# Optimization experiments

Measured on AMD Instinct MI355X. Metric: run time of the kernel, lower is better.

## Reference

```python
import jax, jax.numpy as jnp
import numpy as np

HIDDEN = 1024
HEADS = 8
HEAD = HIDDEN // HEADS
EPS = 1e-5


def _gammas():
    lo = np.log(1.0 / 512.0)
    hi = np.log(1.0 / 32.0)
    lin = np.linspace(lo, hi, HEADS)
    return jnp.asarray(1.0 - np.exp(lin), dtype=jnp.float32)  # [H]


def setup_inputs() -> dict:
    key = jax.random.key(0)
    ks = jax.random.split(key, 7)
    B, S = 2, 2048
    x = jax.random.normal(ks[0], (B, S, HIDDEN), dtype=jnp.float32)
    # Per-head retention projection weights (Retention(head_size, gamma)): [H, d, d]
    Wq = jax.random.normal(ks[1], (HEADS, HEAD, HEAD), dtype=jnp.float32) / HEAD
    Wk = jax.random.normal(ks[2], (HEADS, HEAD, HEAD), dtype=jnp.float32) / HEAD
    Wv = jax.random.normal(ks[3], (HEADS, HEAD, HEAD), dtype=jnp.float32) / HEAD
    W1 = jax.random.normal(ks[4], (HIDDEN, HIDDEN), dtype=jnp.float32) / HIDDEN
    W2 = jax.random.normal(ks[5], (HIDDEN, HIDDEN), dtype=jnp.float32) / HIDDEN
    gn_w = jnp.ones((HIDDEN,), dtype=jnp.float32)
    gn_b = jnp.zeros((HIDDEN,), dtype=jnp.float32)
    return {"x": x, "Wq": Wq, "Wk": Wk, "Wv": Wv, "W1": W1, "W2": W2,
            "gn_w": gn_w, "gn_b": gn_b}


def _decay_mask(S, gammas):
    idx = jnp.arange(S)
    diff = idx[:, None] - idx[None, :]              # [S, S]
    causal = diff >= 0
    safe = jnp.where(causal, diff, 0).astype(jnp.float32)
    D = jnp.where(causal[None], gammas[:, None, None] ** safe[None], 0.0)  # [H,S,S]
    return D


def _msr_forward(x, Wq, Wk, Wv, W1, W2, gn_w, gn_b):
    B, S, _ = x.shape
    xh = x.reshape(B, S, HEADS, HEAD)               # per-head slices
    q = jnp.einsum('bshd,hde->bshe', xh, Wq)
    k = jnp.einsum('bshd,hde->bshe', xh, Wk)
    v = jnp.einsum('bshd,hde->bshe', xh, Wv)
    D = _decay_mask(S, _gammas())                   # [H,S,S]
    scores = jnp.einsum('bnhd,bmhd->bhnm', q, k) * D[None]
    ret = jnp.einsum('bhnm,bmhd->bnhd', scores, v)  # [B,S,H,d]
    # GroupNorm(num_groups=H, channels=HIDDEN) over flattened rows
    mu = jnp.mean(ret, axis=-1, keepdims=True)
    var = jnp.var(ret, axis=-1, keepdims=True)
    ret = (ret - mu) * jax.lax.rsqrt(var + EPS)
    ret = ret.reshape(B, S, HIDDEN) * gn_w + gn_b
    gated = x @ W1
    out = gated * jax.nn.sigmoid(gated) + ret       # swish gate + residual add
    return out @ W2


def reference(x, Wq, Wk, Wv, W1, W2, gn_w, gn_b):
    return _msr_forward(x, Wq, Wk, Wv, W1, W2, gn_w, gn_b)
```

## Files before the change

kernel.cpp:

```cpp
#include <hip/hip_runtime.h>
#include <hip/hip_bf16.h>

#define HID 1024
#define NH 8
#define HD 128
#define BB 2
#define SS 2048
#define CHK 128
#define NCH 16

typedef __attribute__((ext_vector_type(8))) short short8;
typedef __attribute__((ext_vector_type(4))) float f32x4;

static __device__ __forceinline__ float b2f(unsigned short u){
  unsigned int x = ((unsigned int)u) << 16; float f;
  __builtin_memcpy(&f, &x, 4); return f;
}
static __device__ __forceinline__ unsigned short f2b(float f){
  unsigned int x; __builtin_memcpy(&x, &f, 4);
  x += 0x7fffu + ((x >> 16) & 1u);
  return (unsigned short)(x >> 16);
}
static __device__ __forceinline__ float head_gamma(int h){
  double lo = -6.238324625039508;
  double hi = -3.4657359027997265;
  double lin = lo + (hi - lo) * ((double)h / 7.0);
  return (float)(1.0 - exp(lin));
}
static __device__ __forceinline__ f32x4 MFMA(short8 a, short8 b, f32x4 c){
  return __builtin_amdgcn_mfma_f32_16x16x32_bf16(a, b, c, 0, 0, 0);
}

typedef const __attribute__((address_space(1))) unsigned int* gas1_u32p;
typedef __attribute__((address_space(3))) unsigned int* las3_u32p;
static __device__ __forceinline__ void gload_lds16(const void* g, void* l){
  __builtin_amdgcn_global_load_lds((gas1_u32p)g, (las3_u32p)l, 16, 0, 0);
}

__global__ void k_cvt(const float* __restrict__ in, unsigned short* __restrict__ out, int n){
  int i = (blockIdx.x*blockDim.x + threadIdx.x)*4;
  int st = gridDim.x*blockDim.x*4;
  for (; i < n; i += st){
    float4 v = *(const float4*)(in + i);
    unsigned short o[4] = { f2b(v.x), f2b(v.y), f2b(v.z), f2b(v.w) };
    *(uint2*)(out + i) = *(const uint2*)o;
  }
}

__global__ __launch_bounds__(256) void k_wT(const float* __restrict__ in,
                                            unsigned short* __restrict__ out,
                                            int R, int C){
  __shared__ float tile[32][33];
  in  += (size_t)blockIdx.z * R * C;
  out += (size_t)blockIdx.z * R * C;
  int c0 = blockIdx.x*32, r0 = blockIdx.y*32;
  int tx = threadIdx.x & 31, ty = threadIdx.x >> 5;
  #pragma unroll
  for (int i=0;i<4;i++) tile[ty+i*8][tx] = in[(size_t)(r0+ty+i*8)*C + c0+tx];
  __syncthreads();
  #pragma unroll
  for (int i=0;i<4;i++) out[(size_t)(c0+ty+i*8)*R + r0+tx] = f2b(tile[tx][ty+i*8]);
}

__global__ __launch_bounds__(256) void k_qkv(
    const unsigned short* __restrict__ xb,
    const unsigned short* __restrict__ wqT,
    const unsigned short* __restrict__ wkT,
    const unsigned short* __restrict__ wvT,
    unsigned short* __restrict__ qb,
    unsigned short* __restrict__ kb,
    unsigned short* __restrict__ vb)
{
  int bid = blockIdx.x;
  int stile = bid & 31;
  int bh = bid >> 5;
  int h = bh & 7, b = bh >> 3;
  int t = threadIdx.x, wv = t>>6, l = t&63, lr = l&15, lg = l>>4;
  int row0 = stile*64 + wv*16;
  short8 a[4];
  const unsigned short* xp = xb + (size_t)(b*SS + row0 + lr)*HID + h*HD + lg*8;
  #pragma unroll
  for (int kk=0;kk<4;kk++) a[kk] = *(const short8*)(xp + kk*32);
  size_t obase = ((size_t)bh*SS + row0)*HD;
  const unsigned short* wts[3] = { wqT + (size_t)h*HD*HD, wkT + (size_t)h*HD*HD, wvT + (size_t)h*HD*HD };
  unsigned short* outs[3]      = { qb + obase, kb + obase, vb + obase };
  for (int m=0;m<3;m++){
    const unsigned short* wb = wts[m];
    unsigned short* op = outs[m];
    #pragma unroll
    for (int nt=0;nt<8;nt++){
      f32x4 acc = {0.f,0.f,0.f,0.f};
      #pragma unroll
      for (int kk=0;kk<4;kk++){
        short8 bfr = *(const short8*)(wb + (size_t)(nt*16+lr)*HD + kk*32 + lg*8);
        acc = MFMA(a[kk], bfr, acc);
      }
      #pragma unroll
      for (int r=0;r<4;r++)
        op[(size_t)(lg*4+r)*HD + nt*16 + lr] = f2b(acc[r]);
    }
  }
}

__global__ __launch_bounds__(256) void k_chunksum(
    const unsigned short* __restrict__ kb,
    const unsigned short* __restrict__ vb,
    float* __restrict__ U)
{
  int bid = blockIdx.x;
  int c = bid & 15, bh = bid >> 4, h = bh & 7;
  float g = head_gamma(h);
  float l2g = log2f(g);
  __shared__ unsigned short kT[HD][72];
  __shared__ unsigned short vT[HD][72];
  int t = threadIdx.x, wv = t>>6, l = t&63, lr = l&15, lg = l>>4;
  const unsigned short* kc = kb + ((size_t)bh*SS + c*CHK)*HD;
  const unsigned short* vc = vb + ((size_t)bh*SS + c*CHK)*HD;
  f32x4 acc[2][8];
  #pragma unroll
  for (int i=0;i<2;i++)
    #pragma unroll
    for (int j=0;j<8;j++) acc[i][j] = (f32x4){0.f,0.f,0.f,0.f};
  for (int half=0; half<2; half++){
    if (half) __syncthreads();
    #pragma unroll
    for (int it=0; it<4; it++){
      int cid = t + it*256;
      int m = cid >> 4;
      int dc = (cid & 15)*8;
      int mg = half*64 + m;
      short8 kv = *(const short8*)(kc + (size_t)mg*HD + dc);
      short8 vv = *(const short8*)(vc + (size_t)mg*HD + dc);
      float ks = exp2f((float)(CHK-1-mg)*l2g);
      #pragma unroll
      for (int e=0;e<8;e++){
        kT[dc+e][m] = f2b(b2f((unsigned short)kv[e]) * ks);
        vT[dc+e][m] = (unsigned short)vv[e];
      }
    }
    __syncthreads();
    #pragma unroll
    for (int ks=0; ks<2; ks++){
      short8 bfr[8];
      #pragma unroll
      for (int nt=0;nt<8;nt++) bfr[nt] = *(const short8*)&kT[nt*16+lr][ks*32+lg*8];
      #pragma unroll
      for (int mt=0;mt<2;mt++){
        short8 afr = *(const short8*)&vT[wv*32+mt*16+lr][ks*32+lg*8];
        #pragma unroll
        for (int nt=0;nt<8;nt++)
          acc[mt][nt] = MFMA(afr, bfr[nt], acc[mt][nt]);
      }
    }
  }
  float* Up = U + (size_t)bid*HD*HD;
  #pragma unroll
  for (int mt=0;mt<2;mt++)
    #pragma unroll
    for (int nt=0;nt<8;nt++)
      #pragma unroll
      for (int r=0;r<4;r++)
        Up[(size_t)(wv*32+mt*16+lg*4+r)*HD + nt*16+lr] = acc[mt][nt][r];
}

__global__ __launch_bounds__(256) void k_state(
    const float* __restrict__ U,
    unsigned short* __restrict__ ST)
{
  int bid = blockIdx.x;
  int eb = bid & 63, bh = bid >> 6, h = bh & 7;
  float g = head_gamma(h);
  float d128 = exp2f(128.f * log2f(g));
  int idx = eb*256 + threadIdx.x;
  const float* Ub = U + (size_t)bh*NCH*HD*HD + idx;
  unsigned short* Sb = ST + (size_t)bh*NCH*HD*HD + idx;
  float s = 0.f;
  #pragma unroll
  for (int c=0;c<NCH;c++){
    Sb[(size_t)c*HD*HD] = f2b(s);
    s = s*d128 + Ub[(size_t)c*HD*HD];
  }
}

__global__ __launch_bounds__(256) void k_ret(
    const unsigned short* __restrict__ qb,
    const unsigned short* __restrict__ kb,
    const unsigned short* __restrict__ vb,
    const unsigned short* __restrict__ ST,
    const float* __restrict__ gnw,
    const float* __restrict__ gnb,
    unsigned short* __restrict__ ret)
{
  int bid = blockIdx.x;
  int j = bid & 15, bh = bid >> 4, h = bh & 7, b = bh >> 3;
  int p = j*CHK;
  float g = head_gamma(h);
  float l2g = log2f(g);
  __shared__ unsigned short sc[CHK][136];
  __shared__ unsigned short vT[HD][72];
  __shared__ float gpow[CHK];
  int t = threadIdx.x, wv = t>>6, l = t&63, lr = l&15, lg = l>>4;
  if (t < CHK) gpow[t] = exp2f((float)t * l2g);
  const unsigned short* qc = qb + ((size_t)bh*SS + p)*HD;
  const unsigned short* kc = kb + ((size_t)bh*SS + p)*HD;
  const unsigned short* vc = vb + ((size_t)bh*SS + p)*HD;
  const unsigned short* Sp = ST + (size_t)bid*HD*HD;
  __syncthreads();

  auto stageV = [&](int half){
    #pragma unroll
    for (int it=0; it<4; it++){
      int cid = t + it*256;
      int m = cid >> 4;
      int dc = (cid & 15)*8;
      short8 vv = *(const short8*)(vc + (size_t)(half*64 + m)*HD + dc);
      #pragma unroll
      for (int e=0;e<8;e++) vT[dc+e][m] = (unsigned short)vv[e];
    }
  };

  short8 qf[2][4];
  #pragma unroll
  for (int mt=0;mt<2;mt++)
    #pragma unroll
    for (int kk=0;kk<4;kk++)
      qf[mt][kk] = *(const short8*)(qc + (size_t)(wv*32+mt*16+lr)*HD + kk*32 + lg*8);

  #pragma unroll
  for (int nt=0;nt<8;nt++){
    f32x4 a0 = {0,0,0,0}, a1 = {0,0,0,0};
    #pragma unroll
    for (int kk=0;kk<4;kk++){
      short8 bfr = *(const short8*)(kc + (size_t)(nt*16+lr)*HD + kk*32 + lg*8);
      a0 = MFMA(qf[0][kk], bfr, a0);
      a1 = MFMA(qf[1][kk], bfr, a1);
    }
    int col = nt*16 + lr;
    #pragma unroll
    for (int r=0;r<4;r++){
      int r0 = wv*32 + lg*4 + r;
      int r1 = r0 + 16;
      float v0 = (col <= r0) ? a0[r]*gpow[r0-col] : 0.f;
      float v1 = (col <= r1) ? a1[r]*gpow[r1-col] : 0.f;
      sc[r0][col] = f2b(v0);
      sc[r1][col] = f2b(v1);
    }
  }
  stageV(0);
  __syncthreads();

  f32x4 acc[2][8];
  #pragma unroll
  for (int mt=0;mt<2;mt++)
    #pragma unroll
    for (int nt=0;nt<8;nt++){
      f32x4 a = {0,0,0,0};
      #pragma unroll
      for (int kk=0;kk<4;kk++){
        short8 bfr = *(const short8*)(Sp + (size_t)(nt*16+lr)*HD + kk*32 + lg*8);
        a = MFMA(qf[mt][kk], bfr, a);
      }
      acc[mt][nt] = a;
    }
  #pragma unroll
  for (int mt=0;mt<2;mt++)
    #pragma unroll
    for (int r=0;r<4;r++){
      int rr = wv*32 + mt*16 + lg*4 + r;
      float sf = gpow[rr]*g;
      #pragma unroll
      for (int nt=0;nt<8;nt++) acc[mt][nt][r] *= sf;
    }

  for (int half=0; half<2; half++){
    if (half){ __syncthreads(); stageV(1); __syncthreads(); }
    #pragma unroll
    for (int ks=0; ks<2; ks++){
      short8 bfr[8];
      #pragma unroll
      for (int nt=0;nt<8;nt++) bfr[nt] = *(const short8*)&vT[nt*16+lr][ks*32+lg*8];
      #pragma unroll
      for (int mt=0;mt<2;mt++){
        short8 afr = *(const short8*)&sc[wv*32+mt*16+lr][half*64 + ks*32 + lg*8];
        #pragma unroll
        for (int nt=0;nt<8;nt++)
          acc[mt][nt] = MFMA(afr, bfr[nt], acc[mt][nt]);
      }
    }
  }

  unsigned short* rp = ret + ((size_t)(b*SS + p))*HID + h*HD;
  const float* gw  = gnw + h*HD;
  const float* gbb = gnb + h*HD;
  #pragma unroll
  for (int mt=0;mt<2;mt++){
    #pragma unroll
    for (int r=0;r<4;r++){
      float s = 0.f, ss = 0.f;
      #pragma unroll
      for (int nt=0;nt<8;nt++){ float x = acc[mt][nt][r]; s += x; ss += x*x; }
      #pragma unroll
      for (int off=1; off<16; off<<=1){
        s  += __shfl_xor(s,  off, 64);
        ss += __shfl_xor(ss, off, 64);
      }
      float mu  = s*(1.f/128.f);
      float var = ss*(1.f/128.f) - mu*mu;
      float rs  = rsqrtf(var + 1e-5f);
      int rr = wv*32 + mt*16 + lg*4 + r;
      unsigned short* orow = rp + (size_t)rr*HID;
      #pragma unroll
      for (int nt=0;nt<8;nt++){
        int col = nt*16 + lr;
        orow[col] = f2b((acc[mt][nt][r]-mu)*rs*gw[col] + gbb[col]);
      }
    }
  }
}

template<int EPI>
__global__ __launch_bounds__(512) void k_gemm(
    const unsigned short* __restrict__ A,
    const unsigned short* __restrict__ BT,
    const unsigned short* __restrict__ radd,
    unsigned short* __restrict__ Cb,
    float* __restrict__ Cf,
    int M, int N, int K)
{
  __shared__ unsigned short ls[2][2][128*64];
  const int nb = N >> 7;
  const int m0 = (int)(blockIdx.x / nb) << 7;
  const int n0 = (int)(blockIdx.x % nb) << 7;
  const int t = threadIdx.x, wv = t>>6, l = t&63, lr = l&15, lg = l>>4;
  const int wr = (wv>>1)<<5;
  const int wc = (wv&1)<<6;
  const int srow = l >> 3;
  const int sgc  = ((l & 7) ^ srow) << 3;
  const unsigned short* Abase = A  + (size_t)(m0 + wv*16 + srow)*K + sgc;
  const unsigned short* Bbase = BT + (size_t)(n0 + wv*16 + srow)*K + sgc;

  auto stage = [&](int buf, int k0){
    unsigned short* la = &ls[buf][0][0];
    unsigned short* lb = &ls[buf][1][0];
    #pragma unroll
    for (int it=0; it<2; ++it){
      gload_lds16(Abase + (size_t)(it*8)*K + k0, la + (wv*16 + it*8)*64);
      gload_lds16(Bbase + (size_t)(it*8)*K + k0, lb + (wv*16 + it*8)*64);
    }
  };

  f32x4 acc[2][4];
  #pragma unroll
  for (int i=0;i<2;i++)
    #pragma unroll
    for (int j=0;j<4;j++) acc[i][j] = (f32x4){0,0,0,0};

  const int NT = K >> 6;
  stage(0, 0);
  __syncthreads();
  int cur = 0;
  for (int kt = 0; kt < NT; ++kt){
    if (kt+1 < NT) stage(cur^1, (kt+1)<<6);
    const unsigned short* pa = &ls[cur][0][0];
    const unsigned short* pb = &ls[cur][1][0];
    #pragma unroll
    for (int ks=0; ks<2; ++ks){
      short8 af[2], bf[4];
      #pragma unroll
      for (int i=0;i<2;i++){
        int ra = wr + i*16 + lr;
        af[i] = *(const short8*)(pa + ra*64 + ((((ks<<2)+lg) ^ (ra&7))<<3));
      }
      #pragma unroll
      for (int j=0;j<4;j++){
        int rb = wc + j*16 + lr;
        bf[j] = *(const short8*)(pb + rb*64 + ((((ks<<2)+lg) ^ (rb&7))<<3));
      }
      #pragma unroll
      for (int i=0;i<2;i++)
        #pragma unroll
        for (int j=0;j<4;j++)
          acc[i][j] = MFMA(af[i], bf[j], acc[i][j]);
    }
    __syncthreads();
    cur ^= 1;
  }

  #pragma unroll
  for (int i=0;i<2;i++){
    #pragma unroll
    for (int j=0;j<4;j++){
      #pragma unroll
      for (int r=0;r<4;r++){
        int row = m0 + wr + i*16 + lg*4 + r;
        int col = n0 + wc + j*16 + lr;
        float v = acc[i][j][r];
        if (EPI == 1){
          float sw = v / (1.f + __expf(-v));
          Cb[(size_t)row*N + col] = f2b(sw + b2f(radd[(size_t)row*N + col]));
        } else {
          Cf[(size_t)row*N + col] = v;
        }
      }
    }
  }
}

extern "C" void kernel_launch(void* const* d_in, const int* in_sizes, int n_in,
                              void* d_out, int out_size, void* d_ws, size_t ws_size,
                              hipStream_t stream)
{
  (void)in_sizes; (void)n_in; (void)out_size; (void)ws_size;
  const float* x   = (const float*)d_in[0];
  const float* Wq  = (const float*)d_in[1];
  const float* Wk  = (const float*)d_in[2];
  const float* Wv  = (const float*)d_in[3];
  const float* W1  = (const float*)d_in[4];
  const float* W2  = (const float*)d_in[5];
  const float* gnw = (const float*)d_in[6];
  const float* gnb = (const float*)d_in[7];
  float* out = (float*)d_out;

  char* wsp = (char*)d_ws;
  size_t off = 0;
  auto alloc = [&](size_t bytes)->void*{
    off = (off + 255) & ~(size_t)255;
    void* p = wsp + off; off += bytes; return p;
  };
  const size_t NTOK = (size_t)BB*SS;
  unsigned short* xb  = (unsigned short*)alloc(NTOK*HID*2);
  unsigned short* w1T = (unsigned short*)alloc((size_t)HID*HID*2);
  unsigned short* w2T = (unsigned short*)alloc((size_t)HID*HID*2);
  unsigned short* wqT = (unsigned short*)alloc((size_t)NH*HD*HD*2);
  unsigned short* wkT = (unsigned short*)alloc((size_t)NH*HD*HD*2);
  unsigned short* wvT = (unsigned short*)alloc((size_t)NH*HD*HD*2);
  unsigned short* qb  = (unsigned short*)alloc(NTOK*HID*2);
  unsigned short* kb  = (unsigned short*)alloc(NTOK*HID*2);
  unsigned short* vb  = (unsigned short*)alloc(NTOK*HID*2);
  float*          U   = (float*)alloc((size_t)BB*NH*NCH*HD*HD*4);
  unsigned short* ST  = (unsigned short*)alloc((size_t)BB*NH*NCH*HD*HD*2);
  unsigned short* rtb = (unsigned short*)alloc(NTOK*HID*2);
  unsigned short* opb = (unsigned short*)alloc(NTOK*HID*2);

  k_cvt<<<dim3(1024), dim3(256), 0, stream>>>(x, xb, (int)(NTOK*HID));
  k_wT<<<dim3(32,32,1), dim3(256), 0, stream>>>(W1, w1T, HID, HID);
  k_wT<<<dim3(32,32,1), dim3(256), 0, stream>>>(W2, w2T, HID, HID);
  k_wT<<<dim3(4,4,NH), dim3(256), 0, stream>>>(Wq, wqT, HD, HD);
  k_wT<<<dim3(4,4,NH), dim3(256), 0, stream>>>(Wk, wkT, HD, HD);
  k_wT<<<dim3(4,4,NH), dim3(256), 0, stream>>>(Wv, wvT, HD, HD);

  k_qkv<<<dim3(BB*NH*32), dim3(256), 0, stream>>>(xb, wqT, wkT, wvT, qb, kb, vb);
  k_chunksum<<<dim3(BB*NH*NCH), dim3(256), 0, stream>>>(kb, vb, U);
  k_state<<<dim3(BB*NH*64), dim3(256), 0, stream>>>(U, ST);
  k_ret<<<dim3(BB*NH*NCH), dim3(256), 0, stream>>>(qb, kb, vb, ST, gnw, gnb, rtb);

  k_gemm<1><<<dim3(256), dim3(512), 0, stream>>>(xb,  w1T, rtb, opb, nullptr, (int)NTOK, HID, HID);
  k_gemm<2><<<dim3(256), dim3(512), 0, stream>>>(opb, w2T, nullptr, nullptr, out, (int)NTOK, HID, HID);
}
```

Baseline: 122.5 us.

## Emit pre-transposed decayed K and V from QKV kernel, split chunk kernels by halves

The QKV projection now writes K scaled by its intra-chunk decay and V in a transposed per-chunk layout, staged through shared memory. This lets the chunk-sum and retention kernels read MFMA operands straight from global memory instead of transposing through LDS. Both of those kernels are split into two blocks per chunk, which doubles the grid and lets the retention kernel skip the fully masked causal tiles in the first half. The cost is an extra transposed buffer write, a barrier in the QKV kernel, and uncached global operand loads in the chunk kernels.

After: 130.3 us. 6.4% more time.

```diff
diff --git a/kernel.cpp b/kernel.cpp
--- a/kernel.cpp
+++ b/kernel.cpp
@@ -69,24 +69,37 @@
     const unsigned short* __restrict__ wvT,
     unsigned short* __restrict__ qb,
     unsigned short* __restrict__ kb,
-    unsigned short* __restrict__ vb)
+    unsigned short* __restrict__ ktsb,
+    unsigned short* __restrict__ vtb)
 {
   int bid = blockIdx.x;
   int stile = bid & 31;
   int bh = bid >> 5;
   int h = bh & 7, b = bh >> 3;
+  int T0 = stile*64;
+  int chunk = stile >> 1, pm0 = (stile & 1)*64;
+  float l2g = log2f(head_gamma(h));
+  __shared__ unsigned short tl[128*72];
   int t = threadIdx.x, wv = t>>6, l = t&63, lr = l&15, lg = l>>4;
-  int row0 = stile*64 + wv*16;
+  int row0 = T0 + wv*16;
   short8 a[4];
   const unsigned short* xp = xb + (size_t)(b*SS + row0 + lr)*HID + h*HD + lg*8;
   #pragma unroll
   for (int kk=0;kk<4;kk++) a[kk] = *(const short8*)(xp + kk*32);
   size_t obase = ((size_t)bh*SS + row0)*HD;
-  const unsigned short* wts[3] = { wqT + (size_t)h*HD*HD, wkT + (size_t)h*HD*HD, wvT + (size_t)h*HD*HD };
-  unsigned short* outs[3]      = { qb + obase, kb + obase, vb + obase };
-  for (int m=0;m<3;m++){
-    const unsigned short* wb = wts[m];
-    unsigned short* op = outs[m];
+  size_t tbase = ((size_t)(bh*NCH + chunk))*HD*CHK + pm0;
+
+  auto wout = [&](unsigned short* dst){
+    int e = t & 127, th = t >> 7;
+    const uint4* src = (const uint4*)(tl + e*72 + th*32);
+    uint4* d4 = (uint4*)(dst + (size_t)e*CHK + th*32);
+    #pragma unroll
+    for (int i=0;i<4;i++) d4[i] = src[i];
+  };
+
+  {
+    const unsigned short* wb = wqT + (size_t)h*HD*HD;
+    unsigned short* op = qb + obase;
     #pragma unroll
     for (int nt=0;nt<8;nt++){
       f32x4 acc = {0.f,0.f,0.f,0.f};
@@ -100,67 +113,79 @@
         op[(size_t)(lg*4+r)*HD + nt*16 + lr] = f2b(acc[r]);
     }
   }
+  {
+    const unsigned short* wb = wkT + (size_t)h*HD*HD;
+    unsigned short* op = kb + obase;
+    float ksc[4];
+    #pragma unroll
+    for (int r=0;r<4;r++)
+      ksc[r] = exp2f((float)(127 - (pm0 + wv*16 + lg*4 + r))*l2g);
+    #pragma unroll
+    for (int nt=0;nt<8;nt++){
+      f32x4 acc = {0.f,0.f,0.f,0.f};
+      #pragma unroll
+      for (int kk=0;kk<4;kk++){
+        short8 bfr = *(const short8*)(wb + (size_t)(nt*16+lr)*HD + kk*32 + lg*8);
+        acc = MFMA(a[kk], bfr, acc);
+      }
+      #pragma unroll
+      for (int r=0;r<4;r++){
+        op[(size_t)(lg*4+r)*HD + nt*16 + lr] = f2b(acc[r]);
+        tl[(nt*16+lr)*72 + wv*16 + lg*4 + r] = f2b(acc[r]*ksc[r]);
+      }
+    }
+  }
+  __syncthreads();
+  wout(ktsb + tbase);
+  __syncthreads();
+  {
+    const unsigned short* wb = wvT + (size_t)h*HD*HD;
+    #pragma unroll
+    for (int nt=0;nt<8;nt++){
+      f32x4 acc = {0.f,0.f,0.f,0.f};
+      #pragma unroll
+      for (int kk=0;kk<4;kk++){
+        short8 bfr = *(const short8*)(wb + (size_t)(nt*16+lr)*HD + kk*32 + lg*8);
+        acc = MFMA(a[kk], bfr, acc);
+      }
+      #pragma unroll
+      for (int r=0;r<4;r++)
+        tl[(nt*16+lr)*72 + wv*16 + lg*4 + r] = f2b(acc[r]);
+    }
+  }
+  __syncthreads();
+  wout(vtb + tbase);
 }
 
 __global__ __launch_bounds__(256) void k_chunksum(
-    const unsigned short* __restrict__ kb,
-    const unsigned short* __restrict__ vb,
+    const unsigned short* __restrict__ ktsb,
+    const unsigned short* __restrict__ vtb,
     float* __restrict__ U)
 {
   int bid = blockIdx.x;
-  int c = bid & 15, bh = bid >> 4, h = bh & 7;
-  float g = head_gamma(h);
-  float l2g = log2f(g);
-  __shared__ unsigned short kT[HD][72];
-  __shared__ unsigned short vT[HD][72];
+  int eh = bid & 1, cj = bid >> 1;
   int t = threadIdx.x, wv = t>>6, l = t&63, lr = l&15, lg = l>>4;
-  const unsigned short* kc = kb + ((size_t)bh*SS + c*CHK)*HD;
-  const unsigned short* vc = vb + ((size_t)bh*SS + c*CHK)*HD;
-  f32x4 acc[2][8];
-  #pragma unroll
-  for (int i=0;i<2;i++)
-    #pragma unroll
-    for (int j=0;j<8;j++) acc[i][j] = (f32x4){0.f,0.f,0.f,0.f};
-  for (int half=0; half<2; half++){
-    if (half) __syncthreads();
-    #pragma unroll
-    for (int it=0; it<4; it++){
-      int cid = t + it*256;
-      int m = cid >> 4;
-      int dc = (cid & 15)*8;
-      int mg = half*64 + m;
-      short8 kv = *(const short8*)(kc + (size_t)mg*HD + dc);
-      short8 vv = *(const short8*)(vc + (size_t)mg*HD + dc);
-      float ks = exp2f((float)(CHK-1-mg)*l2g);
-      #pragma unroll
-      for (int e=0;e<8;e++){
-        kT[dc+e][m] = f2b(b2f((unsigned short)kv[e]) * ks);
-        vT[dc+e][m] = (unsigned short)vv[e];
-      }
-    }
-    __syncthreads();
-    #pragma unroll
-    for (int ks=0; ks<2; ks++){
-      short8 bfr[8];
-      #pragma unroll
-      for (int nt=0;nt<8;nt++) bfr[nt] = *(const short8*)&kT[nt*16+lr][ks*32+lg*8];
-      #pragma unroll
-      for (int mt=0;mt<2;mt++){
-        short8 afr = *(const short8*)&vT[wv*32+mt*16+lr][ks*32+lg*8];
-        #pragma unroll
-        for (int nt=0;nt<8;nt++)
-          acc[mt][nt] = MFMA(afr, bfr[nt], acc[mt][nt]);
-      }
-    }
-  }
-  float* Up = U + (size_t)bid*HD*HD;
-  #pragma unroll
-  for (int mt=0;mt<2;mt++)
-    #pragma unroll
-    for (int nt=0;nt<8;nt++)
-      #pragma unroll
-      for (int r=0;r<4;r++)
-        Up[(size_t)(wv*32+mt*16+lg*4+r)*HD + nt*16+lr] = acc[mt][nt][r];
+  const unsigned short* vt = vtb  + (size_t)cj*HD*CHK;
+  const unsigned short* kt = ktsb + (size_t)cj*HD*CHK;
+  int e0 = eh*64 + wv*16;
+  f32x4 acc[8];
+  #pragma unroll
+  for (int nt=0;nt<8;nt++) acc[nt] = (f32x4){0.f,0.f,0.f,0.f};
+  #pragma unroll
+  for (int kk=0;kk<4;kk++){
+    short8 afr = *(const short8*)(vt + (size_t)(e0+lr)*CHK + kk*32 + lg*8);
+    #pragma unroll
+    for (int nt=0;nt<8;nt++){
+      short8 bfr = *(const short8*)(kt + (size_t)(nt*16+lr)*CHK + kk*32 + lg*8);
+      acc[nt] = MFMA(afr, bfr, acc[nt]);
+    }
+  }
+  float* Up = U + (size_t)cj*HD*HD;
+  #pragma unroll
+  for (int nt=0;nt<8;nt++)
+    #pragma unroll
+    for (int r=0;r<4;r++)
+      Up[(size_t)(e0+lg*4+r)*HD + nt*16+lr] = acc[nt][r];
 }
 
 __global__ __launch_bounds__(256) void k_state(
@@ -185,135 +210,97 @@
 __global__ __launch_bounds__(256) void k_ret(
     const unsigned short* __restrict__ qb,
     const unsigned short* __restrict__ kb,
-    const unsigned short* __restrict__ vb,
+    const unsigned short* __restrict__ vtb,
     const unsigned short* __restrict__ ST,
     const float* __restrict__ gnw,
     const float* __restrict__ gnb,
     unsigned short* __restrict__ ret)
 {
   int bid = blockIdx.x;
-  int j = bid & 15, bh = bid >> 4, h = bh & 7, b = bh >> 3;
-  int p = j*CHK;
-  float g = head_gamma(h);
-  float l2g = log2f(g);
-  __shared__ unsigned short sc[CHK][136];
-  __shared__ unsigned short vT[HD][72];
-  __shared__ float gpow[CHK];
+  int rh = bid & 1, cj = bid >> 1;
+  int j = cj & 15, bh = cj >> 4, h = bh & 7, b = bh >> 3;
+  int p = j*CHK, rbase = rh*64;
+  float l2g = log2f(head_gamma(h));
+  __shared__ unsigned short sc[64][136];
   int t = threadIdx.x, wv = t>>6, l = t&63, lr = l&15, lg = l>>4;
-  if (t < CHK) gpow[t] = exp2f((float)t * l2g);
   const unsigned short* qc = qb + ((size_t)bh*SS + p)*HD;
   const unsigned short* kc = kb + ((size_t)bh*SS + p)*HD;
-  const unsigned short* vc = vb + ((size_t)bh*SS + p)*HD;
-  const unsigned short* Sp = ST + (size_t)bid*HD*HD;
-  __syncthreads();
-
-  auto stageV = [&](int half){
-    #pragma unroll
-    for (int it=0; it<4; it++){
-      int cid = t + it*256;
-      int m = cid >> 4;
-      int dc = (cid & 15)*8;
-      short8 vv = *(const short8*)(vc + (size_t)(half*64 + m)*HD + dc);
-      #pragma unroll
-      for (int e=0;e<8;e++) vT[dc+e][m] = (unsigned short)vv[e];
-    }
-  };
-
-  short8 qf[2][4];
-  #pragma unroll
-  for (int mt=0;mt<2;mt++)
-    #pragma unroll
-    for (int kk=0;kk<4;kk++)
-      qf[mt][kk] = *(const short8*)(qc + (size_t)(wv*32+mt*16+lr)*HD + kk*32 + lg*8);
-
-  #pragma unroll
-  for (int nt=0;nt<8;nt++){
-    f32x4 a0 = {0,0,0,0}, a1 = {0,0,0,0};
+  const unsigned short* vt = vtb + (size_t)cj*HD*CHK;
+  const unsigned short* Sp = ST + (size_t)cj*HD*HD;
+
+  short8 qf[4];
+  #pragma unroll
+  for (int kk=0;kk<4;kk++)
+    qf[kk] = *(const short8*)(qc + (size_t)(rbase + wv*16 + lr)*HD + kk*32 + lg*8);
+
+  int ntmax = rh ? 8 : 4;
+  for (int nt=0; nt<ntmax; nt++){
+    f32x4 a0 = {0,0,0,0};
     #pragma unroll
     for (int kk=0;kk<4;kk++){
       short8 bfr = *(const short8*)(kc + (size_t)(nt*16+lr)*HD + kk*32 + lg*8);
-      a0 = MFMA(qf[0][kk], bfr, a0);
-      a1 = MFMA(qf[1][kk], bfr, a1);
+      a0 = MFMA(qf[kk], bfr, a0);
     }
     int col = nt*16 + lr;
     #pragma unroll
     for (int r=0;r<4;r++){
-      int r0 = wv*32 + lg*4 + r;
-      int r1 = r0 + 16;
-      float v0 = (col <= r0) ? a0[r]*gpow[r0-col] : 0.f;
-      float v1 = (col <= r1) ? a1[r]*gpow[r1-col] : 0.f;
-      sc[r0][col] = f2b(v0);
-      sc[r1][col] = f2b(v1);
-    }
-  }
-  stageV(0);
-  __syncthreads();
-
-  f32x4 acc[2][8];
-  #pragma unroll
-  for (int mt=0;mt<2;mt++)
-    #pragma unroll
-    for (int nt=0;nt<8;nt++){
-      f32x4 a = {0,0,0,0};
-      #pragma unroll
-      for (int kk=0;kk<4;kk++){
-        short8 bfr = *(const short8*)(Sp + (size_t)(nt*16+lr)*HD + kk*32 + lg*8);
-        a = MFMA(qf[mt][kk], bfr, a);
-      }
-      acc[mt][nt] = a;
-    }
-  #pragma unroll
-  for (int mt=0;mt<2;mt++)
-    #pragma unroll
-    for (int r=0;r<4;r++){
-      int rr = wv*32 + mt*16 + lg*4 + r;
-      float sf = gpow[rr]*g;
-      #pragma unroll
-      for (int nt=0;nt<8;nt++) acc[mt][nt][r] *= sf;
-    }
-
-  for (int half=0; half<2; half++){
-    if (half){ __syncthreads(); stageV(1); __syncthreads(); }
-    #pragma unroll
-    for (int ks=0; ks<2; ks++){
-      short8 bfr[8];
-      #pragma unroll
-      for (int nt=0;nt<8;nt++) bfr[nt] = *(const short8*)&vT[nt*16+lr][ks*32+lg*8];
-      #pragma unroll
-      for (int mt=0;mt<2;mt++){
-        short8 afr = *(const short8*)&sc[wv*32+mt*16+lr][half*64 + ks*32 + lg*8];
-        #pragma unroll
-        for (int nt=0;nt<8;nt++)
-          acc[mt][nt] = MFMA(afr, bfr[nt], acc[mt][nt]);
-      }
-    }
-  }
-
-  unsigned short* rp = ret + ((size_t)(b*SS + p))*HID + h*HD;
+      int n = rbase + wv*16 + lg*4 + r;
+      float v0 = (col <= n) ? a0[r]*exp2f((float)(n-col)*l2g) : 0.f;
+      sc[wv*16 + lg*4 + r][col] = f2b(v0);
+    }
+  }
+
+  f32x4 acc[8];
+  #pragma unroll
+  for (int nt=0;nt<8;nt++){
+    f32x4 aa = {0,0,0,0};
+    #pragma unroll
+    for (int kk=0;kk<4;kk++){
+      short8 bfr = *(const short8*)(Sp + (size_t)(nt*16+lr)*HD + kk*32 + lg*8);
+      aa = MFMA(qf[kk], bfr, aa);
+    }
+    acc[nt] = aa;
+  }
+  #pragma unroll
+  for (int r=0;r<4;r++){
+    int n = rbase + wv*16 + lg*4 + r;
+    float sf = exp2f((float)(n+1)*l2g);
+    #pragma unroll
+    for (int nt=0;nt<8;nt++) acc[nt][r] *= sf;
+  }
+
+  int ksmax = rh ? 4 : 2;
+  for (int ks=0; ks<ksmax; ks++){
+    short8 afr = *(const short8*)&sc[wv*16 + lr][ks*32 + lg*8];
+    #pragma unroll
+    for (int nt=0;nt<8;nt++){
+      short8 bfr = *(const short8*)(vt + (size_t)(nt*16+lr)*CHK + ks*32 + lg*8);
+      acc[nt] = MFMA(afr, bfr, acc[nt]);
+    }
+  }
+
+  unsigned short* rp = ret + ((size_t)(b*SS + p + rbase))*HID + h*HD;
   const float* gw  = gnw + h*HD;
   const float* gbb = gnb + h*HD;
   #pragma unroll
-  for (int mt=0;mt<2;mt++){
-    #pragma unroll
-    for (int r=0;r<4;r++){
-      float s = 0.f, ss = 0.f;
-      #pragma unroll
-      for (int nt=0;nt<8;nt++){ float x = acc[mt][nt][r]; s += x; ss += x*x; }
-      #pragma unroll
-      for (int off=1; off<16; off<<=1){
-        s  += __shfl_xor(s,  off, 64);
-        ss += __shfl_xor(ss, off, 64);
-      }
-      float mu  = s*(1.f/128.f);
-      float var = ss*(1.f/128.f) - mu*mu;
-      float rs  = rsqrtf(var + 1e-5f);
-      int rr = wv*32 + mt*16 + lg*4 + r;
-      unsigned short* orow = rp + (size_t)rr*HID;
-      #pragma unroll
-      for (int nt=0;nt<8;nt++){
-        int col = nt*16 + lr;
-        orow[col] = f2b((acc[mt][nt][r]-mu)*rs*gw[col] + gbb[col]);
-      }
+  for (int r=0;r<4;r++){
+    float s = 0.f, ss = 0.f;
+    #pragma unroll
+    for (int nt=0;nt<8;nt++){ float x = acc[nt][r]; s += x; ss += x*x; }
+    #pragma unroll
+    for (int off=1; off<16; off<<=1){
+      s  += __shfl_xor(s,  off, 64);
+      ss += __shfl_xor(ss, off, 64);
+    }
+    float mu  = s*(1.f/128.f);
+    float var = ss*(1.f/128.f) - mu*mu;
+    float rs  = rsqrtf(var + 1e-5f);
+    int lrow = wv*16 + lg*4 + r;
+    unsigned short* orow = rp + (size_t)lrow*HID;
+    #pragma unroll
+    for (int nt=0;nt<8;nt++){
+      int col = nt*16 + lr;
+      orow[col] = f2b((acc[nt][r]-mu)*rs*gw[col] + gbb[col]);
     }
   }
 }
@@ -428,19 +415,20 @@
     void* p = wsp + off; off += bytes; return p;
   };
   const size_t NTOK = (size_t)BB*SS;
-  unsigned short* xb  = (unsigned short*)alloc(NTOK*HID*2);
-  unsigned short* w1T = (unsigned short*)alloc((size_t)HID*HID*2);
-  unsigned short* w2T = (unsigned short*)alloc((size_t)HID*HID*2);
-  unsigned short* wqT = (unsigned short*)alloc((size_t)NH*HD*HD*2);
-  unsigned short* wkT = (unsigned short*)alloc((size_t)NH*HD*HD*2);
-  unsigned short* wvT = (unsigned short*)alloc((size_t)NH*HD*HD*2);
-  unsigned short* qb  = (unsigned short*)alloc(NTOK*HID*2);
-  unsigned short* kb  = (unsigned short*)alloc(NTOK*HID*2);
-  unsigned short* vb  = (unsigned short*)alloc(NTOK*HID*2);
-  float*          U   = (float*)alloc((size_t)BB*NH*NCH*HD*HD*4);
-  unsigned short* ST  = (unsigned short*)alloc((size_t)BB*NH*NCH*HD*HD*2);
-  unsigned short* rtb = (unsigned short*)alloc(NTOK*HID*2);
-  unsigned short* opb = (unsigned short*)alloc(NTOK*HID*2);
+  unsigned short* xb   = (unsigned short*)alloc(NTOK*HID*2);
+  unsigned short* w1T  = (unsigned short*)alloc((size_t)HID*HID*2);
+  unsigned short* w2T  = (unsigned short*)alloc((size_t)HID*HID*2);
+  unsigned short* wqT  = (unsigned short*)alloc((size_t)NH*HD*HD*2);
+  unsigned short* wkT  = (unsigned short*)alloc((size_t)NH*HD*HD*2);
+  unsigned short* wvT  = (unsigned short*)alloc((size_t)NH*HD*HD*2);
+  unsigned short* qb   = (unsigned short*)alloc(NTOK*HID*2);
+  unsigned short* kb   = (unsigned short*)alloc(NTOK*HID*2);
+  unsigned short* ktsb = (unsigned short*)alloc(NTOK*HID*2);
+  unsigned short* vtb  = (unsigned short*)alloc(NTOK*HID*2);
+  float*          U    = (float*)alloc((size_t)BB*NH*NCH*HD*HD*4);
+  unsigned short* ST   = (unsigned short*)alloc((size_t)BB*NH*NCH*HD*HD*2);
+  unsigned short* rtb  = (unsigned short*)alloc(NTOK*HID*2);
+  unsigned short* opb  = (unsigned short*)alloc(NTOK*HID*2);
 
   k_cvt<<<dim3(1024), dim3(256), 0, stream>>>(x, xb, (int)(NTOK*HID));
   k_wT<<<dim3(32,32,1), dim3(256), 0, stream>>>(W1, w1T, HID, HID);
@@ -449,10 +437,10 @@
   k_wT<<<dim3(4,4,NH), dim3(256), 0, stream>>>(Wk, wkT, HD, HD);
   k_wT<<<dim3(4,4,NH), dim3(256), 0, stream>>>(Wv, wvT, HD, HD);
 
-  k_qkv<<<dim3(BB*NH*32), dim3(256), 0, stream>>>(xb, wqT, wkT, wvT, qb, kb, vb);
-  k_chunksum<<<dim3(BB*NH*NCH), dim3(256), 0, stream>>>(kb, vb, U);
+  k_qkv<<<dim3(BB*NH*32), dim3(256), 0, stream>>>(xb, wqT, wkT, wvT, qb, kb, ktsb, vtb);
+  k_chunksum<<<dim3(BB*NH*NCH*2), dim3(256), 0, stream>>>(ktsb, vtb, U);
   k_state<<<dim3(BB*NH*64), dim3(256), 0, stream>>>(U, ST);
-  k_ret<<<dim3(BB*NH*NCH), dim3(256), 0, stream>>>(qb, kb, vb, ST, gnw, gnb, rtb);
+  k_ret<<<dim3(BB*NH*NCH*2), dim3(256), 0, stream>>>(qb, kb, vtb, ST, gnw, gnb, rtb);
 
   k_gemm<1><<<dim3(256), dim3(512), 0, stream>>>(xb,  w1T, rtb, opb, nullptr, (int)NTOK, HID, HID);
   k_gemm<2><<<dim3(256), dim3(512), 0, stream>>>(opb, w2T, nullptr, nullptr, out, (int)NTOK, HID, HID);
```
